# Kernel tuning notes

Measured on AMD Instinct MI355X. Metric: run time of the kernel, lower is better.

## Reference

```python
import jax, jax.numpy as jnp
import numpy as np

B, N_MM, N_V, N_A = 2, 256, 64, 128
DIM, HEADS, ATTN_RATIO, MLP_RATIO = 1024, 16, 0.25, 4.0
INNER = int(DIM * ATTN_RATIO)          # 256
HID = int(DIM * MLP_RATIO)             # 4096
SCALE = (DIM // HEADS) ** -0.5         # faithful to source: uses dim//num_heads
EPS = 1e-5


def setup_inputs() -> dict:
    key = jax.random.key(0)
    ks = jax.random.split(key, 16)
    s = 0.02
    return {
        "xmm": jax.random.normal(ks[0], (B, N_MM, DIM), jnp.float32),
        "xv": jax.random.normal(ks[1], (B, N_V, DIM), jnp.float32),
        "xa": jax.random.normal(ks[2], (B, N_A, DIM), jnp.float32),
        "ln_mm_w": jnp.ones((DIM,), jnp.float32),
        "ln_mm_b": jnp.zeros((DIM,), jnp.float32),
        "ln_v_w": jnp.ones((DIM,), jnp.float32),
        "ln_v_b": jnp.zeros((DIM,), jnp.float32),
        "ln_a_w": jnp.ones((DIM,), jnp.float32),
        "ln_a_b": jnp.zeros((DIM,), jnp.float32),
        "Wq": jax.random.normal(ks[3], (DIM, INNER), jnp.float32) * s,
        "Wkv": jax.random.normal(ks[4], (2 * DIM, 2 * INNER), jnp.float32) * s,
        "Wproj": jax.random.normal(ks[5], (INNER, DIM), jnp.float32) * s,
        "bproj": jnp.zeros((DIM,), jnp.float32),
        "ln_mlp_w": jnp.ones((DIM,), jnp.float32),
        "ln_mlp_b": jnp.zeros((DIM,), jnp.float32),
        "W1": jax.random.normal(ks[6], (DIM, HID), jnp.float32) * s,
        "b1": jnp.zeros((HID,), jnp.float32),
        "W2": jax.random.normal(ks[7], (HID, DIM), jnp.float32) * s,
        "b2": jnp.zeros((DIM,), jnp.float32),
    }


def _ln(x, w, b):
    m = x.mean(-1, keepdims=True)
    v = ((x - m) ** 2).mean(-1, keepdims=True)
    return (x - m) / jnp.sqrt(v + EPS) * w + b


def reference(xmm, xv, xa, ln_mm_w, ln_mm_b, ln_v_w, ln_v_b, ln_a_w, ln_a_b,
              Wq, Wkv, Wproj, bproj, ln_mlp_w, ln_mlp_b, W1, b1, W2, b2):
    hd = INNER // HEADS
    src_mm = _ln(xmm, ln_mm_w, ln_mm_b)
    src_v = _ln(xv, ln_v_w, ln_v_b)
    src_a = _ln(xa, ln_a_w, ln_a_b)

    # kv(x_va) where x_va = cat([xv broadcast over N_a, xa broadcast over N_v], -1).
    # Equivalent to projecting each stream separately and broadcast-adding:
    kv_v = src_v @ Wkv[:DIM]            # [B, N_v, 2*INNER]
    kv_a = src_a @ Wkv[DIM:]            # [B, N_a, 2*INNER]
    kv = kv_v[:, :, None, :] + kv_a[:, None, :, :]          # [B, N_v, N_a, 2*INNER]
    kv = kv.reshape(B, N_V * N_A, 2, HEADS, hd)
    k = kv[:, :, 0].transpose(0, 2, 1, 3)                   # [B, H, N_va, hd]
    v = kv[:, :, 1].transpose(0, 2, 1, 3)

    q = (src_mm @ Wq).reshape(B, N_MM, HEADS, hd).transpose(0, 2, 1, 3)

    attn = jnp.einsum('bhqd,bhkd->bhqk', q, k) * SCALE
    attn = jax.nn.softmax(attn, axis=-1)
    out = jnp.einsum('bhqk,bhkd->bhqd', attn, v)
    out = out.transpose(0, 2, 1, 3).reshape(B, N_MM, INNER)
    out = out @ Wproj + bproj

    xmm = xmm + out
    h = _ln(xmm, ln_mlp_w, ln_mlp_b)
    h = jax.nn.gelu(h @ W1 + b1, approximate=False) @ W2 + b2
    return xmm + h
```

## Files before the change

kernel.cpp:

```cpp
#include <hip/hip_runtime.h>
#include <hip/hip_bf16.h>
#include <math.h>


typedef unsigned short ushort_t;
typedef __attribute__((ext_vector_type(8))) __bf16 bf16x8;
typedef __attribute__((ext_vector_type(4))) float f32x4;

#define DEVFN static __device__ __forceinline__

DEVFN float bf2f(ushort_t u) {
    return __uint_as_float(((unsigned int)u) << 16);
}
DEVFN ushort_t f2bf(float f) {
    unsigned int x = __float_as_uint(f);
    unsigned int r = x + 0x7FFFu + ((x >> 16) & 1u);
    return (ushort_t)(r >> 16);
}
DEVFN void unpack8(uint4 dv, float* dst) {
    unsigned int ws[4] = {dv.x, dv.y, dv.z, dv.w};
#pragma unroll
    for (int i = 0; i < 4; i++) {
        dst[2 * i] = __uint_as_float(ws[i] << 16);
        dst[2 * i + 1] = __uint_as_float(ws[i] & 0xFFFF0000u);
    }
}

DEVFN void ln_body(const float* __restrict__ x, const float* __restrict__ w,
                   const float* __restrict__ b, ushort_t* __restrict__ out,
                   int row) {
    const float4* xr4 = (const float4*)(x + (size_t)row * 1024);
    ushort_t* orow = out + (size_t)row * 1024;
    int tid = threadIdx.x;
    float4 v4 = xr4[tid];
    float s = v4.x + v4.y + v4.z + v4.w;
    float ss = v4.x * v4.x + v4.y * v4.y + v4.z * v4.z + v4.w * v4.w;
#pragma unroll
    for (int off = 32; off > 0; off >>= 1) {
        s += __shfl_down(s, off);
        ss += __shfl_down(ss, off);
    }
    __shared__ float red[8];
    if ((tid & 63) == 0) {
        red[tid >> 6] = s;
        red[4 + (tid >> 6)] = ss;
    }
    __syncthreads();
    s = red[0] + red[1] + red[2] + red[3];
    ss = red[4] + red[5] + red[6] + red[7];
    float mean = s * (1.f / 1024.f);
    float var = ss * (1.f / 1024.f) - mean * mean;
    float rstd = rsqrtf(var + 1e-5f);
    const float4 w4 = ((const float4*)w)[tid];
    const float4 b4 = ((const float4*)b)[tid];
    union { ushort_t u[4]; uint2 v; } pk;
    pk.u[0] = f2bf((v4.x - mean) * rstd * w4.x + b4.x);
    pk.u[1] = f2bf((v4.y - mean) * rstd * w4.y + b4.y);
    pk.u[2] = f2bf((v4.z - mean) * rstd * w4.z + b4.z);
    pk.u[3] = f2bf((v4.w - mean) * rstd * w4.w + b4.w);
    *(uint2*)(&orow[tid * 4]) = pk.v;
}

__global__ __launch_bounds__(256) void ln_kernel(
    const float* __restrict__ x, const float* __restrict__ w,
    const float* __restrict__ b, ushort_t* __restrict__ out) {
    ln_body(x, w, b, out, blockIdx.x);
}

struct LNSeg {
    const float* x; const float* w; const float* b; ushort_t* out; int start;
};
struct TDesc { const float* in; ushort_t* out; int R, C, nx, start; };

__global__ __launch_bounds__(256) void prep_kernel(LNSeg l0, LNSeg l1,
                                                   LNSeg l2, TDesc d0,
                                                   TDesc d1, TDesc d2,
                                                   TDesc d3, TDesc d4) {
    int id = blockIdx.x;
    if (id < 896) {
        LNSeg s = (id >= l2.start) ? l2 : ((id >= l1.start) ? l1 : l0);
        ln_body(s.x, s.w, s.b, s.out, id - s.start);
        return;
    }
    id -= 896;
    TDesc d = (id >= d4.start) ? d4
            : (id >= d3.start) ? d3
            : (id >= d2.start) ? d2
            : (id >= d1.start) ? d1 : d0;
    int t = id - d.start;
    int bx = (t % d.nx) * 32;
    int by = (t / d.nx) * 32;
    __shared__ ushort_t tile[32][33];
    int tx = threadIdx.x & 31;
    int ty = threadIdx.x >> 5;
    for (int i = ty; i < 32; i += 8)
        tile[i][tx] = f2bf(d.in[(size_t)(by + i) * d.C + bx + tx]);
    __syncthreads();
    for (int i = ty; i < 32; i += 8)
        d.out[(size_t)(bx + i) * d.R + by + tx] = tile[tx][i];
}

template <int EPI, typename OutT>
DEVFN void gemm64_core(const ushort_t* __restrict__ A, int lda,
                       const ushort_t* __restrict__ B, int ldb,
                       OutT* __restrict__ C, int ldc,
                       const float* __restrict__ bias,
                       const float* __restrict__ resid, int K, int m0, int n0,
                       ushort_t* As, ushort_t* Bs) {
    constexpr int LS = 40;
    int tid = threadIdx.x;
    int wave = tid >> 6, lane = tid & 63;
    int wm = wave >> 1, wn = wave & 1;
    int quad = lane >> 4, l16 = lane & 15;

    f32x4 acc[2][2];
#pragma unroll
    for (int i = 0; i < 2; i++)
#pragma unroll
        for (int j = 0; j < 2; j++) acc[i][j] = (f32x4){0.f, 0.f, 0.f, 0.f};

    int r = tid >> 2, c = tid & 3;
    const ushort_t* Ap = A + (size_t)(m0 + r) * lda + c * 8;
    const ushort_t* Bp = B + (size_t)(n0 + r) * ldb + c * 8;
    uint4 ra = *(const uint4*)Ap;
    uint4 rb = *(const uint4*)Bp;

    for (int k0 = 0; k0 < K; k0 += 32) {
        *(uint4*)(&As[r * LS + c * 8]) = ra;
        *(uint4*)(&Bs[r * LS + c * 8]) = rb;
        __syncthreads();
        if (k0 + 32 < K) {
            ra = *(const uint4*)(Ap + k0 + 32);
            rb = *(const uint4*)(Bp + k0 + 32);
        }
        bf16x8 af[2], bfr[2];
#pragma unroll
        for (int i = 0; i < 2; i++)
            af[i] = *(const bf16x8*)(&As[(wm * 32 + i * 16 + l16) * LS + quad * 8]);
#pragma unroll
        for (int j = 0; j < 2; j++)
            bfr[j] = *(const bf16x8*)(&Bs[(wn * 32 + j * 16 + l16) * LS + quad * 8]);
#pragma unroll
        for (int i = 0; i < 2; i++)
#pragma unroll
            for (int j = 0; j < 2; j++)
                acc[i][j] = __builtin_amdgcn_mfma_f32_16x16x32_bf16(
                    af[i], bfr[j], acc[i][j], 0, 0, 0);
        __syncthreads();
    }

#pragma unroll
    for (int i = 0; i < 2; i++)
#pragma unroll
        for (int j = 0; j < 2; j++) {
            int col = n0 + wn * 32 + j * 16 + l16;
            int rbase = m0 + wm * 32 + i * 16 + quad * 4;
            float bv = (EPI == 2 || EPI == 3) ? bias[col] : 0.f;
#pragma unroll
            for (int rr = 0; rr < 4; rr++) {
                int row = rbase + rr;
                float vv = acc[i][j][rr] + bv;
                if (EPI == 2) vv = 0.5f * vv * (1.f + erff(vv * 0.70710678118654752f));
                if (EPI == 3) vv += resid[(size_t)row * ldc + col];
                if constexpr (sizeof(OutT) == 2)
                    C[(size_t)row * ldc + col] = (OutT)f2bf(vv);
                else
                    C[(size_t)row * ldc + col] = vv;
            }
        }
}

template <int EPI, typename OutT>
__global__ __launch_bounds__(256) void gemm64(
    const ushort_t* __restrict__ A, int lda, const ushort_t* __restrict__ Bt,
    int ldb, OutT* __restrict__ C, int ldc, const float* __restrict__ bias,
    const float* __restrict__ resid, int Kper, int sliceStride) {
    __shared__ ushort_t As[64 * 40];
    __shared__ ushort_t Bs[64 * 40];
    int z = blockIdx.z;
    gemm64_core<EPI, OutT>(A + (size_t)z * Kper, lda, Bt + (size_t)z * Kper,
                           ldb, C + (size_t)z * sliceStride, ldc, bias, resid,
                           Kper, blockIdx.y * 64, blockIdx.x * 64, As, Bs);
}

struct GSeg {
    const ushort_t* A; const ushort_t* B; ushort_t* C;
    int lda, ldb, ldc, nx, start;
};
__global__ __launch_bounds__(256) void gemm64_multi(GSeg s0, GSeg s1, GSeg s2,
                                                    int K) {
    __shared__ ushort_t As[64 * 40];
    __shared__ ushort_t Bs[64 * 40];
    int id = blockIdx.x;
    GSeg s = (id >= s2.start) ? s2 : ((id >= s1.start) ? s1 : s0);
    int t = id - s.start;
    int n0 = (t % s.nx) * 64;
    int m0 = (t / s.nx) * 64;
    gemm64_core<0, ushort_t>(s.A, s.lda, s.B, s.ldb, s.C, s.ldc, nullptr,
                             nullptr, K, m0, n0, As, Bs);
}

__global__ __launch_bounds__(256) void reduce_mlp2(
    const float* __restrict__ P, const float* __restrict__ y,
    const float* __restrict__ b2, float* __restrict__ out) {
    int i = blockIdx.x * 256 + threadIdx.x;
    const float4* p = (const float4*)P;
    float4 a = p[i], b = p[i + 131072], cc = p[i + 2 * 131072],
           d = p[i + 3 * 131072];
    float4 yy = ((const float4*)y)[i];
    float4 bb = ((const float4*)b2)[i & 255];
    float4 o;
    o.x = a.x + b.x + cc.x + d.x + yy.x + bb.x;
    o.y = a.y + b.y + cc.y + d.y + yy.y + bb.y;
    o.z = a.z + b.z + cc.z + d.z + yy.z + bb.z;
    o.w = a.w + b.w + cc.w + d.w + yy.w + bb.w;
    ((float4*)out)[i] = o;
}

__global__ __launch_bounds__(256) void attn_kernel(
    const ushort_t* __restrict__ q, const ushort_t* __restrict__ kvv,
    const ushort_t* __restrict__ kva, ushort_t* __restrict__ out) {
    int bh = blockIdx.x;
    int b = bh >> 4, h = bh & 15;
    int tid = threadIdx.x;

    __shared__ float Kv[64][16], Vv[64][16], Ka[128][16], Va[128][16];

    {
        int row = tid >> 2, seg = (tid >> 1) & 1, half = tid & 1;
        const ushort_t* src =
            kvv + (size_t)(b * 64 + row) * 512 + seg * 256 + h * 16 + half * 8;
        float* dst = (seg ? Vv[row] : Kv[row]) + half * 8;
        unpack8(*(const uint4*)src, dst);
    }
#pragma unroll
    for (int t2 = 0; t2 < 2; t2++) {
        int t = tid + t2 * 256;
        int row = t >> 2, seg = (t >> 1) & 1, half = t & 1;
        const ushort_t* src =
            kva + (size_t)(b * 128 + row) * 512 + seg * 256 + h * 16 + half * 8;
        float* dst = (seg ? Va[row] : Ka[row]) + half * 8;
        unpack8(*(const uint4*)src, dst);
    }
    __syncthreads();

    int qlocal = tid >> 2;
    int dg = tid & 3;
    int qrow = blockIdx.y * 64 + qlocal;
    const ushort_t* qp = q + (size_t)(b * 256 + qrow) * 256 + h * 16 + dg * 4;
    uint2 qu = *(const uint2*)qp;
    float4 qv;
    qv.x = __uint_as_float(qu.x << 16) * 0.125f;
    qv.y = __uint_as_float(qu.x & 0xFFFF0000u) * 0.125f;
    qv.z = __uint_as_float(qu.y << 16) * 0.125f;
    qv.w = __uint_as_float(qu.y & 0xFFFF0000u) * 0.125f;

    const float4* Kv4 = (const float4*)Kv;
    const float4* Vv4 = (const float4*)Vv;
    const float4* Ka4 = (const float4*)Ka;
    const float4* Va4 = (const float4*)Va;

    float4 ov = {0.f, 0.f, 0.f, 0.f};
    float den = 0.f;
#pragma unroll 8
    for (int i = 0; i < 64; i++) {
        float4 kk = Kv4[i * 4 + dg];
        float part = qv.x * kk.x + qv.y * kk.y + qv.z * kk.z + qv.w * kk.w;
        part += __shfl_xor(part, 1);
        part += __shfl_xor(part, 2);
        float p = __expf(part);
        den += p;
        float4 vv = Vv4[i * 4 + dg];
        ov.x += p * vv.x; ov.y += p * vv.y; ov.z += p * vv.z; ov.w += p * vv.w;
    }
    float4 oa = {0.f, 0.f, 0.f, 0.f};
    float dena = 0.f;
#pragma unroll 8
    for (int i = 0; i < 128; i++) {
        float4 kk = Ka4[i * 4 + dg];
        float part = qv.x * kk.x + qv.y * kk.y + qv.z * kk.z + qv.w * kk.w;
        part += __shfl_xor(part, 1);
        part += __shfl_xor(part, 2);
        float p = __expf(part);
        dena += p;
        float4 vv = Va4[i * 4 + dg];
        oa.x += p * vv.x; oa.y += p * vv.y; oa.z += p * vv.z; oa.w += p * vv.w;
    }

    float rv = 1.f / den, ra = 1.f / dena;
    union { ushort_t u[4]; uint2 v; } pk;
    pk.u[0] = f2bf(ov.x * rv + oa.x * ra);
    pk.u[1] = f2bf(ov.y * rv + oa.y * ra);
    pk.u[2] = f2bf(ov.z * rv + oa.z * ra);
    pk.u[3] = f2bf(ov.w * rv + oa.w * ra);
    *(uint2*)(out + (size_t)(b * 256 + qrow) * 256 + h * 16 + dg * 4) = pk.v;
}

extern "C" void kernel_launch(void* const* d_in, const int* in_sizes, int n_in,
                              void* d_out, int out_size, void* d_ws,
                              size_t ws_size, hipStream_t stream) {
    const float* xmm = (const float*)d_in[0];
    const float* xv = (const float*)d_in[1];
    const float* xa = (const float*)d_in[2];
    const float* ln_mm_w = (const float*)d_in[3];
    const float* ln_mm_b = (const float*)d_in[4];
    const float* ln_v_w = (const float*)d_in[5];
    const float* ln_v_b = (const float*)d_in[6];
    const float* ln_a_w = (const float*)d_in[7];
    const float* ln_a_b = (const float*)d_in[8];
    const float* Wq = (const float*)d_in[9];
    const float* Wkv = (const float*)d_in[10];
    const float* Wproj = (const float*)d_in[11];
    const float* bproj = (const float*)d_in[12];
    const float* ln_mlp_w = (const float*)d_in[13];
    const float* ln_mlp_b = (const float*)d_in[14];
    const float* W1 = (const float*)d_in[15];
    const float* b1 = (const float*)d_in[16];
    const float* W2 = (const float*)d_in[17];
    const float* b2 = (const float*)d_in[18];
    float* outp = (float*)d_out;

    char* w = (char*)d_ws;
    ushort_t* xmmN = (ushort_t*)w;    w += 512 * 1024 * 2;
    ushort_t* xvN = (ushort_t*)w;     w += 128 * 1024 * 2;
    ushort_t* xaN = (ushort_t*)w;     w += 256 * 1024 * 2;
    ushort_t* Wqt = (ushort_t*)w;     w += 256 * 1024 * 2;
    ushort_t* Wkvt = (ushort_t*)w;    w += 512 * 2048 * 2;
    ushort_t* Wprojt = (ushort_t*)w;  w += 1024 * 256 * 2;
    ushort_t* W1t = (ushort_t*)w;     w += 4096 * 1024 * 2;
    ushort_t* W2t = (ushort_t*)w;     w += 1024 * 4096 * 2;
    ushort_t* qout = (ushort_t*)w;    w += 512 * 256 * 2;
    ushort_t* kvvb = (ushort_t*)w;    w += 128 * 512 * 2;
    ushort_t* kvab = (ushort_t*)w;    w += 256 * 512 * 2;
    ushort_t* attnout = (ushort_t*)w; w += 512 * 256 * 2;
    float* y = (float*)w;             w += 512 * 1024 * 4;
    ushort_t* h0 = (ushort_t*)w;      w += 512 * 1024 * 2;
    ushort_t* g = (ushort_t*)w;       w += 512 * 4096 * 2;
    float* P = (float*)w;             w += 4 * 512 * 1024 * 4;

    LNSeg L0{xmm, ln_mm_w, ln_mm_b, xmmN, 0};
    LNSeg L1{xv, ln_v_w, ln_v_b, xvN, 512};
    LNSeg L2{xa, ln_a_w, ln_a_b, xaN, 640};
    TDesc T0{Wq, Wqt, 1024, 256, 8, 0};
    TDesc T1{Wkv, Wkvt, 2048, 512, 16, 256};
    TDesc T2{Wproj, Wprojt, 256, 1024, 32, 1280};
    TDesc T3{W1, W1t, 1024, 4096, 128, 1536};
    TDesc T4{W2, W2t, 4096, 1024, 32, 5632};
    prep_kernel<<<896 + 9728, 256, 0, stream>>>(L0, L1, L2, T0, T1, T2, T3, T4);

    GSeg G0{xmmN, Wqt, qout, 1024, 1024, 256, 4, 0};
    GSeg G1{xvN, Wkvt, kvvb, 1024, 2048, 512, 8, 32};
    GSeg G2{xaN, Wkvt + 1024, kvab, 1024, 2048, 512, 8, 48};
    gemm64_multi<<<80, 256, 0, stream>>>(G0, G1, G2, 1024);

    attn_kernel<<<dim3(32, 4), 256, 0, stream>>>(qout, kvvb, kvab, attnout);

    gemm64<3, float><<<dim3(16, 8, 1), 256, 0, stream>>>(
        attnout, 256, Wprojt, 256, y, 1024, bproj, xmm, 256, 0);

    ln_kernel<<<512, 256, 0, stream>>>(y, ln_mlp_w, ln_mlp_b, h0);

    gemm64<2, ushort_t><<<dim3(64, 8, 1), 256, 0, stream>>>(
        h0, 1024, W1t, 1024, g, 4096, b1, nullptr, 1024, 0);

    gemm64<4, float><<<dim3(16, 8, 4), 256, 0, stream>>>(
        g, 4096, W2t, 4096, P, 1024, nullptr, nullptr, 1024, 512 * 1024);

    reduce_mlp2<<<512, 256, 0, stream>>>(P, y, b2, outp);

    (void)in_sizes; (void)n_in; (void)out_size; (void)ws_size;
}
```

Measured before the change: 202.1 us.

## Fuse MLP layernorm into W1 GEMM and replace split-K reduce with atomics

The projection GEMM now writes y and also initialises the output buffer with y + b2. The MLP layernorm is computed inside the W1 GEMM: each block computes row statistics from y and normalises the A tile on the fly, so the separate LN kernel and h0 buffer go away. The split-K W2 GEMM atomically adds its partial sums into the output, which removes the partial buffer and the reduce kernel. In exchange, each of the 64 column blocks recomputes the row statistics, and float atomics make the summation order nondeterministic.

```diff
diff --git a/kernel.cpp b/kernel.cpp
--- a/kernel.cpp
+++ b/kernel.cpp
@@ -59,12 +59,6 @@
     pk.u[2] = f2bf((v4.z - mean) * rstd * w4.z + b4.z);
     pk.u[3] = f2bf((v4.w - mean) * rstd * w4.w + b4.w);
     *(uint2*)(&orow[tid * 4]) = pk.v;
-}
-
-__global__ __launch_bounds__(256) void ln_kernel(
-    const float* __restrict__ x, const float* __restrict__ w,
-    const float* __restrict__ b, ushort_t* __restrict__ out) {
-    ln_body(x, w, b, out, blockIdx.x);
 }
 
 struct LNSeg {
@@ -106,7 +100,9 @@
                        OutT* __restrict__ C, int ldc,
                        const float* __restrict__ bias,
                        const float* __restrict__ resid, int K, int m0, int n0,
-                       ushort_t* As, ushort_t* Bs) {
+                       ushort_t* As, ushort_t* Bs,
+                       const float* __restrict__ bias2 = nullptr,
+                       float* __restrict__ out2 = nullptr) {
     constexpr int LS = 40;
     int tid = threadIdx.x;
     int wave = tid >> 6, lane = tid & 63;
@@ -155,17 +151,21 @@
         for (int j = 0; j < 2; j++) {
             int col = n0 + wn * 32 + j * 16 + l16;
             int rbase = m0 + wm * 32 + i * 16 + quad * 4;
-            float bv = (EPI == 2 || EPI == 3) ? bias[col] : 0.f;
+            float bv = (EPI == 6) ? bias[col] : 0.f;
+            float bv2 = (EPI == 6) ? bias2[col] : 0.f;
 #pragma unroll
             for (int rr = 0; rr < 4; rr++) {
                 int row = rbase + rr;
                 float vv = acc[i][j][rr] + bv;
-                if (EPI == 2) vv = 0.5f * vv * (1.f + erff(vv * 0.70710678118654752f));
-                if (EPI == 3) vv += resid[(size_t)row * ldc + col];
-                if constexpr (sizeof(OutT) == 2)
+                if (EPI == 6) {
+                    vv += resid[(size_t)row * ldc + col];
+                    C[(size_t)row * ldc + col] = vv;
+                    out2[(size_t)row * ldc + col] = vv + bv2;
+                } else if (EPI == 5) {
+                    atomicAdd((float*)&C[(size_t)row * ldc + col], vv);
+                } else {
                     C[(size_t)row * ldc + col] = (OutT)f2bf(vv);
-                else
-                    C[(size_t)row * ldc + col] = vv;
+                }
             }
         }
 }
@@ -200,21 +200,124 @@
                              nullptr, K, m0, n0, As, Bs);
 }
 
-__global__ __launch_bounds__(256) void reduce_mlp2(
-    const float* __restrict__ P, const float* __restrict__ y,
-    const float* __restrict__ b2, float* __restrict__ out) {
-    int i = blockIdx.x * 256 + threadIdx.x;
-    const float4* p = (const float4*)P;
-    float4 a = p[i], b = p[i + 131072], cc = p[i + 2 * 131072],
-           d = p[i + 3 * 131072];
-    float4 yy = ((const float4*)y)[i];
-    float4 bb = ((const float4*)b2)[i & 255];
-    float4 o;
-    o.x = a.x + b.x + cc.x + d.x + yy.x + bb.x;
-    o.y = a.y + b.y + cc.y + d.y + yy.y + bb.y;
-    o.z = a.z + b.z + cc.z + d.z + yy.z + bb.z;
-    o.w = a.w + b.w + cc.w + d.w + yy.w + bb.w;
-    ((float4*)out)[i] = o;
+__global__ __launch_bounds__(256) void ygemm_kernel(
+    const ushort_t* __restrict__ A, const ushort_t* __restrict__ Bt,
+    float* __restrict__ y, const float* __restrict__ bproj,
+    const float* __restrict__ xmm, const float* __restrict__ b2,
+    float* __restrict__ out0) {
+    __shared__ ushort_t As[64 * 40];
+    __shared__ ushort_t Bs[64 * 40];
+    gemm64_core<6, float>(A, 256, Bt, 256, y, 1024, bproj, xmm, 256,
+                          blockIdx.y * 64, blockIdx.x * 64, As, Bs, b2, out0);
+}
+
+__global__ __launch_bounds__(256) void mlp1_kernel(
+    const float* __restrict__ y, const float* __restrict__ lnw,
+    const float* __restrict__ lnb, const ushort_t* __restrict__ W1t,
+    const float* __restrict__ b1, ushort_t* __restrict__ g) {
+    constexpr int LS = 40;
+    __shared__ ushort_t As[64 * LS];
+    __shared__ ushort_t Bs[64 * LS];
+    __shared__ float meanv[64], rstdv[64];
+    __shared__ float wls[1024], bls[1024];
+    int tid = threadIdx.x;
+    int m0 = blockIdx.y * 64, n0 = blockIdx.x * 64;
+
+    ((float4*)wls)[tid] = ((const float4*)lnw)[tid];
+    ((float4*)bls)[tid] = ((const float4*)lnb)[tid];
+
+    {
+        int rr = tid >> 2, q = tid & 3;
+        const float4* yr = (const float4*)(y + (size_t)(m0 + rr) * 1024) + q * 64;
+        float s = 0.f, ss = 0.f;
+#pragma unroll 8
+        for (int i = 0; i < 64; i++) {
+            float4 v = yr[i];
+            s += v.x + v.y + v.z + v.w;
+            ss += v.x * v.x + v.y * v.y + v.z * v.z + v.w * v.w;
+        }
+        s += __shfl_xor(s, 1); ss += __shfl_xor(ss, 1);
+        s += __shfl_xor(s, 2); ss += __shfl_xor(ss, 2);
+        if (q == 0) {
+            float mean = s * (1.f / 1024.f);
+            float var = ss * (1.f / 1024.f) - mean * mean;
+            meanv[rr] = mean;
+            rstdv[rr] = rsqrtf(var + 1e-5f);
+        }
+    }
+    __syncthreads();
+
+    int wave = tid >> 6, lane = tid & 63;
+    int wm = wave >> 1, wn = wave & 1;
+    int quad = lane >> 4, l16 = lane & 15;
+
+    f32x4 acc[2][2];
+#pragma unroll
+    for (int i = 0; i < 2; i++)
+#pragma unroll
+        for (int j = 0; j < 2; j++) acc[i][j] = (f32x4){0.f, 0.f, 0.f, 0.f};
+
+    int r = tid >> 2, c = tid & 3;
+    const float* Ay = y + (size_t)(m0 + r) * 1024 + c * 8;
+    const ushort_t* Bp = W1t + (size_t)(n0 + r) * 1024 + c * 8;
+    float mr = meanv[r], rs = rstdv[r];
+    float4 ya0 = *(const float4*)Ay;
+    float4 ya1 = *(const float4*)(Ay + 4);
+    uint4 rb = *(const uint4*)Bp;
+
+    for (int k0 = 0; k0 < 1024; k0 += 32) {
+        float4 w0 = *(const float4*)&wls[k0 + c * 8];
+        float4 w1 = *(const float4*)&wls[k0 + c * 8 + 4];
+        float4 bb0 = *(const float4*)&bls[k0 + c * 8];
+        float4 bb1 = *(const float4*)&bls[k0 + c * 8 + 4];
+        union { ushort_t u[8]; uint4 v; } pa;
+        pa.u[0] = f2bf((ya0.x - mr) * rs * w0.x + bb0.x);
+        pa.u[1] = f2bf((ya0.y - mr) * rs * w0.y + bb0.y);
+        pa.u[2] = f2bf((ya0.z - mr) * rs * w0.z + bb0.z);
+        pa.u[3] = f2bf((ya0.w - mr) * rs * w0.w + bb0.w);
+        pa.u[4] = f2bf((ya1.x - mr) * rs * w1.x + bb1.x);
+        pa.u[5] = f2bf((ya1.y - mr) * rs * w1.y + bb1.y);
+        pa.u[6] = f2bf((ya1.z - mr) * rs * w1.z + bb1.z);
+        pa.u[7] = f2bf((ya1.w - mr) * rs * w1.w + bb1.w);
+        *(uint4*)(&As[r * LS + c * 8]) = pa.v;
+        *(uint4*)(&Bs[r * LS + c * 8]) = rb;
+        __syncthreads();
+        if (k0 + 32 < 1024) {
+            ya0 = *(const float4*)(Ay + k0 + 32);
+            ya1 = *(const float4*)(Ay + k0 + 36);
+            rb = *(const uint4*)(Bp + k0 + 32);
+        }
+        bf16x8 af[2], bfr[2];
+#pragma unroll
+        for (int i = 0; i < 2; i++)
+            af[i] = *(const bf16x8*)(&As[(wm * 32 + i * 16 + l16) * LS + quad * 8]);
+#pragma unroll
+        for (int j = 0; j < 2; j++)
+            bfr[j] = *(const bf16x8*)(&Bs[(wn * 32 + j * 16 + l16) * LS + quad * 8]);
+#pragma unroll
+        for (int i = 0; i < 2; i++)
+#pragma unroll
+            for (int j = 0; j < 2; j++)
+                acc[i][j] = __builtin_amdgcn_mfma_f32_16x16x32_bf16(
+                    af[i], bfr[j], acc[i][j], 0, 0, 0);
+        __syncthreads();
+    }
+
+#pragma unroll
+    for (int i = 0; i < 2; i++)
+#pragma unroll
+        for (int j = 0; j < 2; j++) {
+            int col = n0 + wn * 32 + j * 16 + l16;
+            int rbase = m0 + wm * 32 + i * 16 + quad * 4;
+            float bv = b1[col];
+#pragma unroll
+            for (int rr = 0; rr < 4; rr++) {
+                int row = rbase + rr;
+                float vv = acc[i][j][rr] + bv;
+                vv = 0.5f * vv * (1.f + erff(vv * 0.70710678118654752f));
+                g[(size_t)row * 4096 + col] = f2bf(vv);
+            }
+        }
 }
 
 __global__ __launch_bounds__(256) void attn_kernel(
@@ -334,9 +437,7 @@
     ushort_t* kvab = (ushort_t*)w;    w += 256 * 512 * 2;
     ushort_t* attnout = (ushort_t*)w; w += 512 * 256 * 2;
     float* y = (float*)w;             w += 512 * 1024 * 4;
-    ushort_t* h0 = (ushort_t*)w;      w += 512 * 1024 * 2;
     ushort_t* g = (ushort_t*)w;       w += 512 * 4096 * 2;
-    float* P = (float*)w;             w += 4 * 512 * 1024 * 4;
 
     LNSeg L0{xmm, ln_mm_w, ln_mm_b, xmmN, 0};
     LNSeg L1{xv, ln_v_w, ln_v_b, xvN, 512};
@@ -355,18 +456,14 @@
 
     attn_kernel<<<dim3(32, 4), 256, 0, stream>>>(qout, kvvb, kvab, attnout);
 
-    gemm64<3, float><<<dim3(16, 8, 1), 256, 0, stream>>>(
-        attnout, 256, Wprojt, 256, y, 1024, bproj, xmm, 256, 0);
-
-    ln_kernel<<<512, 256, 0, stream>>>(y, ln_mlp_w, ln_mlp_b, h0);
-
-    gemm64<2, ushort_t><<<dim3(64, 8, 1), 256, 0, stream>>>(
-        h0, 1024, W1t, 1024, g, 4096, b1, nullptr, 1024, 0);
-
-    gemm64<4, float><<<dim3(16, 8, 4), 256, 0, stream>>>(
-        g, 4096, W2t, 4096, P, 1024, nullptr, nullptr, 1024, 512 * 1024);
-
-    reduce_mlp2<<<512, 256, 0, stream>>>(P, y, b2, outp);
+    ygemm_kernel<<<dim3(16, 8), 256, 0, stream>>>(attnout, Wprojt, y, bproj,
+                                                  xmm, b2, outp);
+
+    mlp1_kernel<<<dim3(64, 8), 256, 0, stream>>>(y, ln_mlp_w, ln_mlp_b, W1t,
+                                                 b1, g);
+
+    gemm64<5, float><<<dim3(16, 8, 4), 256, 0, stream>>>(
+        g, 4096, W2t, 4096, outp, 1024, nullptr, nullptr, 1024, 0);
 
     (void)in_sizes; (void)n_in; (void)out_size; (void)ws_size;
 }
```

Result: slower. 213.2 us (+5.5%).

## Overlap weight transposes with QKV projection and double GEMM K-tile to 64

Applied to the files above, without the earlier changes.

Moves the Wproj, W1 and W2 fp32-to-bf16 transposes out of the prep kernel and into the same launch as the small Q/KV projection GEMM. The 80 GEMM blocks, which would otherwise leave most CUs idle, now run alongside the transpose blocks. The shared GEMM core also changes from 32-wide to 64-wide K tiles, with padded LDS rows of 72, which halves the number of barrier pairs per K loop. The cost is more LDS and registers per block, which may reduce occupancy.

```diff
diff --git a/kernel.cpp b/kernel.cpp
--- a/kernel.cpp
+++ b/kernel.cpp
@@ -9,9 +9,6 @@
 
 #define DEVFN static __device__ __forceinline__
 
-DEVFN float bf2f(ushort_t u) {
-    return __uint_as_float(((unsigned int)u) << 16);
-}
 DEVFN ushort_t f2bf(float f) {
     unsigned int x = __float_as_uint(f);
     unsigned int r = x + 0x7FFFu + ((x >> 16) & 1u);
@@ -72,25 +69,9 @@
 };
 struct TDesc { const float* in; ushort_t* out; int R, C, nx, start; };
 
-__global__ __launch_bounds__(256) void prep_kernel(LNSeg l0, LNSeg l1,
-                                                   LNSeg l2, TDesc d0,
-                                                   TDesc d1, TDesc d2,
-                                                   TDesc d3, TDesc d4) {
-    int id = blockIdx.x;
-    if (id < 896) {
-        LNSeg s = (id >= l2.start) ? l2 : ((id >= l1.start) ? l1 : l0);
-        ln_body(s.x, s.w, s.b, s.out, id - s.start);
-        return;
-    }
-    id -= 896;
-    TDesc d = (id >= d4.start) ? d4
-            : (id >= d3.start) ? d3
-            : (id >= d2.start) ? d2
-            : (id >= d1.start) ? d1 : d0;
-    int t = id - d.start;
+DEVFN void transpose_body(TDesc d, int t, ushort_t (*tile)[33]) {
     int bx = (t % d.nx) * 32;
     int by = (t / d.nx) * 32;
-    __shared__ ushort_t tile[32][33];
     int tx = threadIdx.x & 31;
     int ty = threadIdx.x >> 5;
     for (int i = ty; i < 32; i += 8)
@@ -100,6 +81,21 @@
         d.out[(size_t)(bx + i) * d.R + by + tx] = tile[tx][i];
 }
 
+__global__ __launch_bounds__(256) void prep_kernel(LNSeg l0, LNSeg l1,
+                                                   LNSeg l2, TDesc d0,
+                                                   TDesc d1) {
+    int id = blockIdx.x;
+    if (id < 896) {
+        LNSeg s = (id >= l2.start) ? l2 : ((id >= l1.start) ? l1 : l0);
+        ln_body(s.x, s.w, s.b, s.out, id - s.start);
+        return;
+    }
+    id -= 896;
+    __shared__ ushort_t tile[32][33];
+    TDesc d = (id >= d1.start) ? d1 : d0;
+    transpose_body(d, id - d.start, tile);
+}
+
 template <int EPI, typename OutT>
 DEVFN void gemm64_core(const ushort_t* __restrict__ A, int lda,
                        const ushort_t* __restrict__ B, int ldb,
@@ -107,7 +103,7 @@
                        const float* __restrict__ bias,
                        const float* __restrict__ resid, int K, int m0, int n0,
                        ushort_t* As, ushort_t* Bs) {
-    constexpr int LS = 40;
+    constexpr int LS = 72;
     int tid = threadIdx.x;
     int wave = tid >> 6, lane = tid & 63;
     int wm = wave >> 1, wn = wave & 1;
@@ -119,33 +115,45 @@
 #pragma unroll
         for (int j = 0; j < 2; j++) acc[i][j] = (f32x4){0.f, 0.f, 0.f, 0.f};
 
-    int r = tid >> 2, c = tid & 3;
+    int r = tid >> 3;
+    int c = tid & 7;
     const ushort_t* Ap = A + (size_t)(m0 + r) * lda + c * 8;
     const ushort_t* Bp = B + (size_t)(n0 + r) * ldb + c * 8;
-    uint4 ra = *(const uint4*)Ap;
-    uint4 rb = *(const uint4*)Bp;
-
-    for (int k0 = 0; k0 < K; k0 += 32) {
+    const ushort_t* Ap2 = Ap + (size_t)32 * lda;
+    const ushort_t* Bp2 = Bp + (size_t)32 * ldb;
+    uint4 ra = *(const uint4*)Ap, ra2 = *(const uint4*)Ap2;
+    uint4 rb = *(const uint4*)Bp, rb2 = *(const uint4*)Bp2;
+
+    for (int k0 = 0; k0 < K; k0 += 64) {
         *(uint4*)(&As[r * LS + c * 8]) = ra;
+        *(uint4*)(&As[(r + 32) * LS + c * 8]) = ra2;
         *(uint4*)(&Bs[r * LS + c * 8]) = rb;
+        *(uint4*)(&Bs[(r + 32) * LS + c * 8]) = rb2;
         __syncthreads();
-        if (k0 + 32 < K) {
-            ra = *(const uint4*)(Ap + k0 + 32);
-            rb = *(const uint4*)(Bp + k0 + 32);
+        if (k0 + 64 < K) {
+            ra = *(const uint4*)(Ap + k0 + 64);
+            ra2 = *(const uint4*)(Ap2 + k0 + 64);
+            rb = *(const uint4*)(Bp + k0 + 64);
+            rb2 = *(const uint4*)(Bp2 + k0 + 64);
         }
-        bf16x8 af[2], bfr[2];
-#pragma unroll
-        for (int i = 0; i < 2; i++)
-            af[i] = *(const bf16x8*)(&As[(wm * 32 + i * 16 + l16) * LS + quad * 8]);
-#pragma unroll
-        for (int j = 0; j < 2; j++)
-            bfr[j] = *(const bf16x8*)(&Bs[(wn * 32 + j * 16 + l16) * LS + quad * 8]);
-#pragma unroll
-        for (int i = 0; i < 2; i++)
+#pragma unroll
+        for (int ks = 0; ks < 2; ks++) {
+            bf16x8 af[2], bfr[2];
+#pragma unroll
+            for (int i = 0; i < 2; i++)
+                af[i] = *(const bf16x8*)(
+                    &As[(wm * 32 + i * 16 + l16) * LS + ks * 32 + quad * 8]);
 #pragma unroll
             for (int j = 0; j < 2; j++)
-                acc[i][j] = __builtin_amdgcn_mfma_f32_16x16x32_bf16(
-                    af[i], bfr[j], acc[i][j], 0, 0, 0);
+                bfr[j] = *(const bf16x8*)(
+                    &Bs[(wn * 32 + j * 16 + l16) * LS + ks * 32 + quad * 8]);
+#pragma unroll
+            for (int i = 0; i < 2; i++)
+#pragma unroll
+                for (int j = 0; j < 2; j++)
+                    acc[i][j] = __builtin_amdgcn_mfma_f32_16x16x32_bf16(
+                        af[i], bfr[j], acc[i][j], 0, 0, 0);
+        }
         __syncthreads();
     }
 
@@ -175,8 +183,8 @@
     const ushort_t* __restrict__ A, int lda, const ushort_t* __restrict__ Bt,
     int ldb, OutT* __restrict__ C, int ldc, const float* __restrict__ bias,
     const float* __restrict__ resid, int Kper, int sliceStride) {
-    __shared__ ushort_t As[64 * 40];
-    __shared__ ushort_t Bs[64 * 40];
+    __shared__ ushort_t As[64 * 72];
+    __shared__ ushort_t Bs[64 * 72];
     int z = blockIdx.z;
     gemm64_core<EPI, OutT>(A + (size_t)z * Kper, lda, Bt + (size_t)z * Kper,
                            ldb, C + (size_t)z * sliceStride, ldc, bias, resid,
@@ -187,17 +195,25 @@
     const ushort_t* A; const ushort_t* B; ushort_t* C;
     int lda, ldb, ldc, nx, start;
 };
-__global__ __launch_bounds__(256) void gemm64_multi(GSeg s0, GSeg s1, GSeg s2,
-                                                    int K) {
-    __shared__ ushort_t As[64 * 40];
-    __shared__ ushort_t Bs[64 * 40];
+
+__global__ __launch_bounds__(256) void projT_kernel(GSeg s0, GSeg s1, GSeg s2,
+                                                    TDesc d0, TDesc d1,
+                                                    TDesc d2, int K) {
+    __shared__ ushort_t As[64 * 72];
+    __shared__ ushort_t Bs[64 * 72];
     int id = blockIdx.x;
-    GSeg s = (id >= s2.start) ? s2 : ((id >= s1.start) ? s1 : s0);
-    int t = id - s.start;
-    int n0 = (t % s.nx) * 64;
-    int m0 = (t / s.nx) * 64;
-    gemm64_core<0, ushort_t>(s.A, s.lda, s.B, s.ldb, s.C, s.ldc, nullptr,
-                             nullptr, K, m0, n0, As, Bs);
+    if (id < 80) {
+        GSeg s = (id >= s2.start) ? s2 : ((id >= s1.start) ? s1 : s0);
+        int t = id - s.start;
+        int n0 = (t % s.nx) * 64;
+        int m0 = (t / s.nx) * 64;
+        gemm64_core<0, ushort_t>(s.A, s.lda, s.B, s.ldb, s.C, s.ldc, nullptr,
+                                 nullptr, K, m0, n0, As, Bs);
+        return;
+    }
+    id -= 80;
+    TDesc d = (id >= d2.start) ? d2 : ((id >= d1.start) ? d1 : d0);
+    transpose_body(d, id - d.start, (ushort_t(*)[33])As);
 }
 
 __global__ __launch_bounds__(256) void reduce_mlp2(
@@ -341,17 +357,17 @@
     LNSeg L0{xmm, ln_mm_w, ln_mm_b, xmmN, 0};
     LNSeg L1{xv, ln_v_w, ln_v_b, xvN, 512};
     LNSeg L2{xa, ln_a_w, ln_a_b, xaN, 640};
-    TDesc T0{Wq, Wqt, 1024, 256, 8, 0};
-    TDesc T1{Wkv, Wkvt, 2048, 512, 16, 256};
-    TDesc T2{Wproj, Wprojt, 256, 1024, 32, 1280};
-    TDesc T3{W1, W1t, 1024, 4096, 128, 1536};
-    TDesc T4{W2, W2t, 4096, 1024, 32, 5632};
-    prep_kernel<<<896 + 9728, 256, 0, stream>>>(L0, L1, L2, T0, T1, T2, T3, T4);
+    TDesc TQ{Wq, Wqt, 1024, 256, 8, 0};
+    TDesc TKV{Wkv, Wkvt, 2048, 512, 16, 256};
+    prep_kernel<<<896 + 1280, 256, 0, stream>>>(L0, L1, L2, TQ, TKV);
 
     GSeg G0{xmmN, Wqt, qout, 1024, 1024, 256, 4, 0};
     GSeg G1{xvN, Wkvt, kvvb, 1024, 2048, 512, 8, 32};
     GSeg G2{xaN, Wkvt + 1024, kvab, 1024, 2048, 512, 8, 48};
-    gemm64_multi<<<80, 256, 0, stream>>>(G0, G1, G2, 1024);
+    TDesc TP{Wproj, Wprojt, 256, 1024, 32, 0};
+    TDesc T1{W1, W1t, 1024, 4096, 128, 256};
+    TDesc T2{W2, W2t, 4096, 1024, 32, 4352};
+    projT_kernel<<<80 + 8448, 256, 0, stream>>>(G0, G1, G2, TP, T1, T2, 1024);
 
     attn_kernel<<<dim3(32, 4), 256, 0, stream>>>(qout, kvvb, kvab, attnout);
 
```

New measurement: 187.4 us. 1.08x faster.
